# Kernel optimization log

Hardware: AMD Instinct MI355X
Metric: run time of the kernel (lower is better)

## Reference

```python
import jax, jax.numpy as jnp
import numpy as np

D = 768      # d_model (hardcoded in module)
H = 12       # heads (ViT-Base)
HD = D // H  # head_dim = 64
FF = 4 * D   # mlp hidden = 3072
L = 32       # num_latents
B, N = 64, 197
EPS = 1e-6


def _ln(x, g, b):
    mu = jnp.mean(x, axis=-1, keepdims=True)
    var = jnp.mean(jnp.square(x - mu), axis=-1, keepdims=True)
    return (x - mu) * jax.lax.rsqrt(var + EPS) * g + b


def _attn_simple(q, k, v):
    # fusion attention: single-head, scale = C ** -0.5 over full dim
    C = q.shape[-1]
    a = jax.nn.softmax(jnp.einsum('bnc,bmc->bnm', q, k) * (C ** -0.5), axis=-1)
    return jnp.einsum('bnm,bmc->bnc', a, v)


def _mha(x, qkv_w, qkv_b, proj_w, proj_b):
    Bx, Nx, C = x.shape
    qkv = (x @ qkv_w + qkv_b).reshape(Bx, Nx, 3, H, HD)
    q, k, v = jnp.moveaxis(qkv, 2, 0)           # each [B, N, H, HD]
    scores = jnp.einsum('bnhd,bmhd->bhnm', q, k) * (HD ** -0.5)
    a = jax.nn.softmax(scores, axis=-1)
    out = jnp.einsum('bhnm,bmhd->bnhd', a, v).reshape(Bx, Nx, C)
    return out @ proj_w + proj_b


def _mlp(x, w1, b1, w2, b2):
    return jax.nn.gelu(x @ w1 + b1, approximate=False) @ w2 + b2


def setup_inputs() -> dict:
    key = jax.random.key(0)
    ks = iter(jax.random.split(key, 40))
    std = 0.02
    d = {
        'x': jax.random.normal(next(ks), (B, N, D), jnp.float32),
        'y': jax.random.normal(next(ks), (B, N, D), jnp.float32),
        'latents': jax.random.normal(next(ks), (1, L, D), jnp.float32) * std,
        'scale_a': jnp.zeros((1,), jnp.float32) + 0.1,
        'scale_v': jnp.zeros((1,), jnp.float32) + 0.1,
    }
    for p in ('p', 'm'):
        d[f'{p}_n1_g'] = jnp.ones((D,), jnp.float32)
        d[f'{p}_n1_b'] = jnp.zeros((D,), jnp.float32)
        d[f'{p}_qkv_w'] = jax.random.normal(next(ks), (D, 3 * D), jnp.float32) * std
        d[f'{p}_qkv_b'] = jnp.zeros((3 * D,), jnp.float32)
        d[f'{p}_proj_w'] = jax.random.normal(next(ks), (D, D), jnp.float32) * std
        d[f'{p}_proj_b'] = jnp.zeros((D,), jnp.float32)
        d[f'{p}_n2_g'] = jnp.ones((D,), jnp.float32)
        d[f'{p}_n2_b'] = jnp.zeros((D,), jnp.float32)
        d[f'{p}_fc1_w'] = jax.random.normal(next(ks), (D, FF), jnp.float32) * std
        d[f'{p}_fc1_b'] = jnp.zeros((FF,), jnp.float32)
        d[f'{p}_fc2_w'] = jax.random.normal(next(ks), (FF, D), jnp.float32) * std
        d[f'{p}_fc2_b'] = jnp.zeros((D,), jnp.float32)
    return d


def reference(x, y, latents, scale_a, scale_v,
              p_n1_g, p_n1_b, p_qkv_w, p_qkv_b, p_proj_w, p_proj_b,
              p_n2_g, p_n2_b, p_fc1_w, p_fc1_b, p_fc2_w, p_fc2_b,
              m_n1_g, m_n1_b, m_qkv_w, m_qkv_b, m_proj_w, m_proj_b,
              m_n2_g, m_n2_b, m_fc1_w, m_fc1_b, m_fc2_w, m_fc2_b):
    BS = x.shape[0]
    # ---- fusion: latent bottleneck cross-attention ----
    concat = jnp.concatenate([x, y], axis=1)                       # [B, 2N, D]
    lat = jnp.broadcast_to(latents, (BS, L, D))
    fused = _attn_simple(lat, concat, concat)                      # [B, L, D]
    x = x + scale_a * _attn_simple(x, fused, fused)
    y = y + scale_v * _attn_simple(y, fused, fused)
    # ---- pre-norm attn + MLP blocks ----
    x = x + _mha(_ln(x, p_n1_g, p_n1_b), p_qkv_w, p_qkv_b, p_proj_w, p_proj_b)
    y = y + _mha(_ln(y, m_n1_g, m_n1_b), m_qkv_w, m_qkv_b, m_proj_w, m_proj_b)
    x = x + _mlp(_ln(x, p_n2_g, p_n2_b), p_fc1_w, p_fc1_b, p_fc2_w, p_fc2_b)
    y = y + _mlp(_ln(y, m_n2_g, m_n2_b), m_fc1_w, m_fc1_b, m_fc2_w, m_fc2_b)
    return (x, y)
```

## Files before the change

### kernel.cpp

```cpp
#include <hip/hip_runtime.h>
#include <math.h>


namespace {

constexpr int BB = 64, NN = 197, DD = 768, HH = 12, HDIM = 64, FF = 3072, LL = 32;
constexpr int N2 = 2 * NN;
constexpr int ROWS = BB * NN;
constexpr float SCALE_D = 0.036084391824351615f;
constexpr float SCALE_H = 0.125f;

constexpr long long B_AHI    = 0;
constexpr long long B_ALO    = 19365888;
constexpr long long B_GHI    = 40894464;
constexpr long long B_GLO    = 118358016;
constexpr long long B_CONCAT = 0;
constexpr long long B_SCORES = 0;
constexpr long long B_QKV    = 125829120;
constexpr long long B_FUSED  = 242221056;
constexpr long long B_S1T    = 248512512;
constexpr long long B_A2     = 252706816;
constexpr long long B_S2     = 256901120;
constexpr long long B_P1     = 258998272;
constexpr long long B_WHI    = 297795584;
constexpr long long B_WLO    = 303038464;

__device__ inline ushort f2bf(float f) {
  unsigned x = __float_as_uint(f);
  unsigned r = (x + 0x7FFFu + ((x >> 16) & 1u)) >> 16;
  return (ushort)r;
}
__device__ inline float bf2f(ushort u) {
  return __uint_as_float(((unsigned)u) << 16);
}

using bf16x8v = __attribute__((ext_vector_type(8))) short;
using f32x4v  = __attribute__((ext_vector_type(4))) float;

enum { ME_BIAS = 0, ME_RESID_BIAS = 1, ME_GELU_SPLIT = 2 };

struct MP {
  const ushort* Ah; const ushort* Al; int lda;
  const ushort* Wh; const ushort* Wl; int ldw;
  float* C; int ldc;
  const float* bias;
  const float* R; int ldr;
  ushort* Oh; ushort* Ol; int ldo;
  int M, N, K;
};

template <int EPI>
__global__ __launch_bounds__(256, 2) void mgemm_k(MP p) {
  __shared__ ushort sAh[128 * 40], sAl[128 * 40], sBh[128 * 40], sBl[128 * 40];
  const int tid = threadIdx.x;
  const int m0 = blockIdx.y * 128, n0 = blockIdx.x * 128;
  const int l = tid & 63, w = tid >> 6;
  const int wm = (w >> 1) * 64, wn = (w & 1) * 64;
  const int fr = l & 15, fq = l >> 4;

  f32x4v acc[4][4];
#pragma unroll
  for (int i = 0; i < 4; ++i)
#pragma unroll
    for (int j = 0; j < 4; ++j)
#pragma unroll
      for (int r = 0; r < 4; ++r) acc[i][j][r] = 0.f;

  const int srow = tid >> 2;
  const int skg  = tid & 3;

  for (int k0 = 0; k0 < p.K; k0 += 32) {
#pragma unroll
    for (int pass = 0; pass < 2; ++pass) {
      const int row = srow + pass * 64;
      const int lo_off = row * 40 + skg * 8;
      {
        const int mg = m0 + row;
        uint4 vh = make_uint4(0, 0, 0, 0), vl = make_uint4(0, 0, 0, 0);
        if (mg < p.M) {
          const long long off = (long long)mg * p.lda + k0 + skg * 8;
          vh = *reinterpret_cast<const uint4*>(p.Ah + off);
          vl = *reinterpret_cast<const uint4*>(p.Al + off);
        }
        *reinterpret_cast<uint4*>(&sAh[lo_off]) = vh;
        *reinterpret_cast<uint4*>(&sAl[lo_off]) = vl;
      }
      {
        const int ng = n0 + row;
        const long long off = (long long)ng * p.ldw + k0 + skg * 8;
        *reinterpret_cast<uint4*>(&sBh[lo_off]) =
            *reinterpret_cast<const uint4*>(p.Wh + off);
        *reinterpret_cast<uint4*>(&sBl[lo_off]) =
            *reinterpret_cast<const uint4*>(p.Wl + off);
      }
    }
    __syncthreads();

    bf16x8v ah[4], al[4];
#pragma unroll
    for (int mi = 0; mi < 4; ++mi) {
      const int ro = (wm + mi * 16 + fr) * 40 + fq * 8;
      ah[mi] = *reinterpret_cast<const bf16x8v*>(&sAh[ro]);
      al[mi] = *reinterpret_cast<const bf16x8v*>(&sAl[ro]);
    }
#pragma unroll
    for (int ni = 0; ni < 4; ++ni) {
      const int ro = (wn + ni * 16 + fr) * 40 + fq * 8;
      const bf16x8v bh = *reinterpret_cast<const bf16x8v*>(&sBh[ro]);
      const bf16x8v bl = *reinterpret_cast<const bf16x8v*>(&sBl[ro]);
#pragma unroll
      for (int mi = 0; mi < 4; ++mi) {
        acc[mi][ni] = __builtin_amdgcn_mfma_f32_16x16x32_bf16(al[mi], bh, acc[mi][ni], 0, 0, 0);
        acc[mi][ni] = __builtin_amdgcn_mfma_f32_16x16x32_bf16(ah[mi], bl, acc[mi][ni], 0, 0, 0);
        acc[mi][ni] = __builtin_amdgcn_mfma_f32_16x16x32_bf16(ah[mi], bh, acc[mi][ni], 0, 0, 0);
      }
    }
    __syncthreads();
  }

#pragma unroll
  for (int mi = 0; mi < 4; ++mi) {
    const int rb = m0 + wm + mi * 16 + fq * 4;
#pragma unroll
    for (int ni = 0; ni < 4; ++ni) {
      const int col = n0 + wn + ni * 16 + fr;
#pragma unroll
      for (int r = 0; r < 4; ++r) {
        const int mg = rb + r;
        if (mg >= p.M) continue;
        float v = acc[mi][ni][r];
        if (EPI == ME_BIAS) {
          p.C[(long long)mg * p.ldc + col] = v + p.bias[col];
        } else if (EPI == ME_RESID_BIAS) {
          p.C[(long long)mg * p.ldc + col] =
              v + p.bias[col] + p.R[(long long)mg * p.ldr + col];
        } else {
          v += p.bias[col];
          v = 0.5f * v * (1.f + erff(v * 0.70710678118654752f));
          const ushort h = f2bf(v);
          const long long o = (long long)mg * p.ldo + col;
          p.Oh[o] = h;
          p.Ol[o] = f2bf(v - bf2f(h));
        }
      }
    }
  }
}

template <int EPI>
static void launch_mgemm(hipStream_t st, const MP& p) {
  dim3 grid(p.N / 128, (p.M + 127) / 128);
  hipLaunchKernelGGL(HIP_KERNEL_NAME(mgemm_k<EPI>), grid, dim3(256), 0, st, p);
}

struct GemmP {
  const float* A; long long sA1, sA2; int lda;
  const float* W; long long sW1, sW2; int ldw;
  float*       C; long long sC1, sC2; int ldc;
  const float* R; long long sR1, sR2; int ldr;
  const float* bias;
  const float* scaleptr;
  int M, N, K, Z2;
  float alpha;
};

enum { E_NONE = 0, E_BIAS = 1, E_RESID_SCALE = 4 };

template <int BM, int BN, int BK, int TM, int TN, bool WT, int EPI>
__global__ __launch_bounds__(256) void gemm_k(GemmP p) {
  constexpr int NX = BN / TN;
  __shared__ float As[BK][BM + 4];
  __shared__ float Ws[BK][BN + 4];

  const int tid = threadIdx.x;
  const int z = blockIdx.z;
  const int z1 = z / p.Z2, z2 = z % p.Z2;
  const float* A = p.A + (long long)z1 * p.sA1 + (long long)z2 * p.sA2;
  const float* W = p.W + (long long)z1 * p.sW1 + (long long)z2 * p.sW2;
  float*       C = p.C + (long long)z1 * p.sC1 + (long long)z2 * p.sC2;
  const float* R = p.R ? p.R + (long long)z1 * p.sR1 + (long long)z2 * p.sR2 : nullptr;

  const int m0 = blockIdx.y * BM;
  const int n0 = blockIdx.x * BN;
  const int tx = tid % NX;
  const int ty = tid / NX;

  float acc[TM][TN];
#pragma unroll
  for (int i = 0; i < TM; ++i)
#pragma unroll
    for (int j = 0; j < TN; ++j) acc[i][j] = 0.f;

  for (int k0 = 0; k0 < p.K; k0 += BK) {
    for (int l = tid; l < BM * BK; l += 256) {
      const int m = l / BK, kc = l % BK;
      const int mg = m0 + m, kg = k0 + kc;
      float v = 0.f;
      if (mg < p.M && kg < p.K) v = A[(long long)mg * p.lda + kg];
      As[kc][m] = v;
    }
    if (!WT) {
      for (int l = tid; l < BK * BN; l += 256) {
        const int kc = l / BN, n = l % BN;
        const int ng = n0 + n, kg = k0 + kc;
        float v = 0.f;
        if (ng < p.N && kg < p.K) v = W[(long long)kg * p.ldw + ng];
        Ws[kc][n] = v;
      }
    } else {
      for (int l = tid; l < BK * BN; l += 256) {
        const int n = l / BK, kc = l % BK;
        const int ng = n0 + n, kg = k0 + kc;
        float v = 0.f;
        if (ng < p.N && kg < p.K) v = W[(long long)ng * p.ldw + kg];
        Ws[kc][n] = v;
      }
    }
    __syncthreads();

#pragma unroll
    for (int kk = 0; kk < BK; ++kk) {
      float af[TM], wf[TN];
#pragma unroll
      for (int i = 0; i < TM; i += 4) {
        const float4 t = *reinterpret_cast<const float4*>(&As[kk][ty * TM + i]);
        af[i] = t.x; af[i + 1] = t.y; af[i + 2] = t.z; af[i + 3] = t.w;
      }
#pragma unroll
      for (int j = 0; j < TN; j += 4) {
        const float4 t = *reinterpret_cast<const float4*>(&Ws[kk][tx * TN + j]);
        wf[j] = t.x; wf[j + 1] = t.y; wf[j + 2] = t.z; wf[j + 3] = t.w;
      }
#pragma unroll
      for (int i = 0; i < TM; ++i)
#pragma unroll
        for (int j = 0; j < TN; ++j) acc[i][j] += af[i] * wf[j];
    }
    __syncthreads();
  }

  float sc = 0.f;
  if (EPI == E_RESID_SCALE) sc = p.scaleptr[0];
#pragma unroll
  for (int i = 0; i < TM; ++i) {
    const int mg = m0 + ty * TM + i;
    if (mg >= p.M) continue;
#pragma unroll
    for (int j = 0; j < TN; ++j) {
      const int ng = n0 + tx * TN + j;
      if (ng >= p.N) continue;
      float v = acc[i][j];
      if (EPI == E_NONE) v *= p.alpha;
      if (EPI == E_BIAS) v += p.bias[ng];
      if (EPI == E_RESID_SCALE) v = R[(long long)mg * p.ldr + ng] + sc * v;
      C[(long long)mg * p.ldc + ng] = v;
    }
  }
}

template <int BM, int BN, int BK, int TM, int TN, bool WT, int EPI>
static void launch_gemm(hipStream_t st, const GemmP& p, int Z) {
  dim3 grid((p.N + BN - 1) / BN, (p.M + BM - 1) / BM, Z);
  hipLaunchKernelGGL(HIP_KERNEL_NAME(gemm_k<BM, BN, BK, TM, TN, WT, EPI>),
                     grid, dim3(256), 0, st, p);
}


__global__ __launch_bounds__(256) void concat_k(const float* __restrict__ x,
                                                const float* __restrict__ y,
                                                float* __restrict__ c) {
  const long long total4 = (long long)BB * N2 * DD / 4;
  const long long i = (long long)blockIdx.x * 256 + threadIdx.x;
  if (i >= total4) return;
  const long long e = i * 4;
  const int b = (int)(e / ((long long)N2 * DD));
  const long long rem = e % ((long long)N2 * DD);
  const int r = (int)(rem / DD);
  const int col = (int)(rem % DD);
  const float* src = (r < NN) ? (x + ((long long)b * NN + r) * DD + col)
                              : (y + ((long long)b * NN + (r - NN)) * DD + col);
  reinterpret_cast<float4*>(c)[i] = *reinterpret_cast<const float4*>(src);
}

__global__ __launch_bounds__(256) void ln_split_k(const float* __restrict__ in,
                                                  ushort* __restrict__ oh,
                                                  ushort* __restrict__ ol,
                                                  const float* __restrict__ g,
                                                  const float* __restrict__ b) {
  const int row = blockIdx.x;
  const int tid = threadIdx.x;
  const float* src = in + (long long)row * DD;
  const float v0 = src[tid], v1 = src[tid + 256], v2 = src[tid + 512];
  __shared__ float red[4];
  const int wid = tid >> 6;

  float s = v0 + v1 + v2;
#pragma unroll
  for (int o = 32; o; o >>= 1) s += __shfl_xor(s, o);
  if ((tid & 63) == 0) red[wid] = s;
  __syncthreads();
  const float mu = (red[0] + red[1] + red[2] + red[3]) * (1.f / 768.f);
  const float d0 = v0 - mu, d1 = v1 - mu, d2 = v2 - mu;
  __syncthreads();

  float q = d0 * d0 + d1 * d1 + d2 * d2;
#pragma unroll
  for (int o = 32; o; o >>= 1) q += __shfl_xor(q, o);
  if ((tid & 63) == 0) red[wid] = q;
  __syncthreads();
  const float var = (red[0] + red[1] + red[2] + red[3]) * (1.f / 768.f);
  const float rs = 1.f / sqrtf(var + 1e-6f);

  ushort* dh = oh + (long long)row * DD;
  ushort* dl = ol + (long long)row * DD;
#pragma unroll
  for (int c = 0; c < 3; ++c) {
    const int idx = tid + c * 256;
    const float dv = (c == 0 ? d0 : c == 1 ? d1 : d2);
    const float v = dv * rs * g[idx] + b[idx];
    const ushort h = f2bf(v);
    dh[idx] = h;
    dl[idx] = f2bf(v - bf2f(h));
  }
}

__global__ __launch_bounds__(256) void split_k(const float* __restrict__ in,
                                               ushort* __restrict__ oh,
                                               ushort* __restrict__ ol,
                                               long long n4) {
  const long long i = (long long)blockIdx.x * 256 + threadIdx.x;
  if (i >= n4) return;
  const float4 v = reinterpret_cast<const float4*>(in)[i];
  ushort4 h, lo;
  h.x = f2bf(v.x); lo.x = f2bf(v.x - bf2f(h.x));
  h.y = f2bf(v.y); lo.y = f2bf(v.y - bf2f(h.y));
  h.z = f2bf(v.z); lo.z = f2bf(v.z - bf2f(h.z));
  h.w = f2bf(v.w); lo.w = f2bf(v.w - bf2f(h.w));
  reinterpret_cast<ushort4*>(oh)[i] = h;
  reinterpret_cast<ushort4*>(ol)[i] = lo;
}

__global__ __launch_bounds__(256) void wsplit_k(const float* __restrict__ W,
                                                ushort* __restrict__ th,
                                                ushort* __restrict__ tl,
                                                int K, int N) {
  __shared__ float t[32][33];
  const int tid = threadIdx.x;
  const int kb = blockIdx.y * 32, nb = blockIdx.x * 32;
  for (int u = tid; u < 1024; u += 256) {
    const int k = u >> 5, n = u & 31;
    t[k][n] = W[(long long)(kb + k) * N + nb + n];
  }
  __syncthreads();
  const int n = tid >> 3, k4 = tid & 7;
  ushort4 vh, vl;
  {
    float v;
    v = t[k4 * 4 + 0][n]; vh.x = f2bf(v); vl.x = f2bf(v - bf2f(vh.x));
    v = t[k4 * 4 + 1][n]; vh.y = f2bf(v); vl.y = f2bf(v - bf2f(vh.y));
    v = t[k4 * 4 + 2][n]; vh.z = f2bf(v); vl.z = f2bf(v - bf2f(vh.z));
    v = t[k4 * 4 + 3][n]; vh.w = f2bf(v); vl.w = f2bf(v - bf2f(vh.w));
  }
  const long long o = (long long)(nb + n) * K + kb + k4 * 4;
  *reinterpret_cast<ushort4*>(th + o) = vh;
  *reinterpret_cast<ushort4*>(tl + o) = vl;
}

__global__ __launch_bounds__(256) void sm1_k(const float* __restrict__ S1t,
                                             float* __restrict__ A2) {
  const int b = blockIdx.x >> 5, l = blockIdx.x & 31;
  const int tid = threadIdx.x;
  const float* src = S1t + (long long)b * N2 * LL + l;
  const bool has2 = (tid + 256) < N2;
  const float v0 = src[(long long)tid * LL];
  const float v1 = has2 ? src[(long long)(tid + 256) * LL] : -3.0e38f;

  __shared__ float red[4];
  const int wid = tid >> 6;
  float mx = fmaxf(v0, v1);
#pragma unroll
  for (int o = 32; o; o >>= 1) mx = fmaxf(mx, __shfl_xor(mx, o));
  if ((tid & 63) == 0) red[wid] = mx;
  __syncthreads();
  mx = fmaxf(fmaxf(red[0], red[1]), fmaxf(red[2], red[3]));
  __syncthreads();

  const float p0 = expf(v0 - mx);
  const float p1 = has2 ? expf(v1 - mx) : 0.f;
  float s = p0 + p1;
#pragma unroll
  for (int o = 32; o; o >>= 1) s += __shfl_xor(s, o);
  if ((tid & 63) == 0) red[wid] = s;
  __syncthreads();
  const float inv = 1.f / (red[0] + red[1] + red[2] + red[3]);

  float* dst = A2 + (long long)b * LL * N2 + (long long)l * N2;
  dst[tid] = p0 * inv;
  if (has2) dst[tid + 256] = p1 * inv;
}

__global__ __launch_bounds__(256) void sm2_k(float* __restrict__ S, int rows) {
  const long long i = (long long)blockIdx.x * 256 + threadIdx.x;
  if (i >= rows) return;
  float* r = S + i * 32;
  float v[32];
  const float4* r4 = reinterpret_cast<const float4*>(r);
#pragma unroll
  for (int j = 0; j < 8; ++j) {
    const float4 t = r4[j];
    v[4 * j] = t.x; v[4 * j + 1] = t.y; v[4 * j + 2] = t.z; v[4 * j + 3] = t.w;
  }
  float mx = v[0];
#pragma unroll
  for (int j = 1; j < 32; ++j) mx = fmaxf(mx, v[j]);
  float s = 0.f;
#pragma unroll
  for (int j = 0; j < 32; ++j) { v[j] = expf(v[j] - mx); s += v[j]; }
  const float inv = 1.f / s;
  float4* w4 = reinterpret_cast<float4*>(r);
#pragma unroll
  for (int j = 0; j < 8; ++j) {
    float4 t;
    t.x = v[4 * j] * inv; t.y = v[4 * j + 1] * inv;
    t.z = v[4 * j + 2] * inv; t.w = v[4 * j + 3] * inv;
    w4[j] = t;
  }
}

__global__ __launch_bounds__(256) void smS_k(float* __restrict__ S, long long rows) {
  const int lane = threadIdx.x & 63;
  const long long row = (long long)blockIdx.x * 4 + (threadIdx.x >> 6);
  if (row >= rows) return;
  float* r = S + row * NN;
  float v[4];
#pragma unroll
  for (int j = 0; j < 4; ++j) {
    const int idx = lane + j * 64;
    v[j] = (idx < NN) ? r[idx] : -3.0e38f;
  }
  float mx = fmaxf(fmaxf(v[0], v[1]), fmaxf(v[2], v[3]));
#pragma unroll
  for (int o = 32; o; o >>= 1) mx = fmaxf(mx, __shfl_xor(mx, o));
  float pv[4];
  float s = 0.f;
#pragma unroll
  for (int j = 0; j < 4; ++j) {
    const int idx = lane + j * 64;
    pv[j] = (idx < NN) ? expf(v[j] - mx) : 0.f;
    s += pv[j];
  }
#pragma unroll
  for (int o = 32; o; o >>= 1) s += __shfl_xor(s, o);
  const float inv = 1.f / s;
#pragma unroll
  for (int j = 0; j < 4; ++j) {
    const int idx = lane + j * 64;
    if (idx < NN) r[idx] = pv[j] * inv;
  }
}

static GemmP mk(const float* A, long long sA1, long long sA2, int lda,
                const float* W, long long sW1, long long sW2, int ldw,
                float* C, long long sC1, long long sC2, int ldc,
                int M, int N, int K, int Z2, float alpha,
                const float* bias = nullptr,
                const float* R = nullptr, long long sR1 = 0, long long sR2 = 0, int ldr = 0,
                const float* scaleptr = nullptr) {
  GemmP p;
  p.A = A; p.sA1 = sA1; p.sA2 = sA2; p.lda = lda;
  p.W = W; p.sW1 = sW1; p.sW2 = sW2; p.ldw = ldw;
  p.C = C; p.sC1 = sC1; p.sC2 = sC2; p.ldc = ldc;
  p.R = R; p.sR1 = sR1; p.sR2 = sR2; p.ldr = ldr;
  p.bias = bias; p.scaleptr = scaleptr;
  p.M = M; p.N = N; p.K = K; p.Z2 = Z2; p.alpha = alpha;
  return p;
}

static MP mkm(const ushort* Ah, const ushort* Al, int lda,
              const ushort* Wh, const ushort* Wl, int ldw,
              int M, int N, int K, const float* bias,
              float* C = nullptr, int ldc = 0,
              const float* R = nullptr, int ldr = 0,
              ushort* Oh = nullptr, ushort* Ol = nullptr, int ldo = 0) {
  MP p;
  p.Ah = Ah; p.Al = Al; p.lda = lda;
  p.Wh = Wh; p.Wl = Wl; p.ldw = ldw;
  p.C = C; p.ldc = ldc; p.bias = bias;
  p.R = R; p.ldr = ldr;
  p.Oh = Oh; p.Ol = Ol; p.ldo = ldo;
  p.M = M; p.N = N; p.K = K;
  return p;
}

}

extern "C" void kernel_launch(void* const* d_in, const int* in_sizes, int n_in,
                              void* d_out, int out_size, void* d_ws, size_t ws_size,
                              hipStream_t stream) {
  const float* x   = (const float*)d_in[0];
  const float* y   = (const float*)d_in[1];
  const float* lat = (const float*)d_in[2];
  const float* scale_a = (const float*)d_in[3];
  const float* scale_v = (const float*)d_in[4];
  const float* PRM[2][12];
  for (int i = 0; i < 12; ++i) {
    PRM[0][i] = (const float*)d_in[5 + i];
    PRM[1][i] = (const float*)d_in[17 + i];
  }

  char* ws = (char*)d_ws;
  ushort* Ahi = (ushort*)(ws + B_AHI);
  ushort* Alo = (ushort*)(ws + B_ALO);
  ushort* Ghi = (ushort*)(ws + B_GHI);
  ushort* Glo = (ushort*)(ws + B_GLO);
  float* concat = (float*)(ws + B_CONCAT);
  float* scores = (float*)(ws + B_SCORES);
  float* qkv    = (float*)(ws + B_QKV);
  float* fused  = (float*)(ws + B_FUSED);
  float* S1t    = (float*)(ws + B_S1T);
  float* A2     = (float*)(ws + B_A2);
  float* S2     = (float*)(ws + B_S2);
  float* P1     = (float*)(ws + B_P1);
  ushort* Whi   = (ushort*)(ws + B_WHI);
  ushort* Wlo   = (ushort*)(ws + B_WLO);

  float* outX = (float*)d_out;
  float* outY = outX + (long long)ROWS * DD;

  {
    const long long tot4 = (long long)BB * N2 * DD / 4;
    concat_k<<<(unsigned)((tot4 + 255) / 256), 256, 0, stream>>>(x, y, concat);
  }
  launch_gemm<128, 32, 8, 4, 4, true, E_NONE>(
      stream,
      mk(concat, (long long)N2 * DD, 0, DD,
         lat, 0, 0, DD,
         S1t, (long long)N2 * LL, 0, LL,
         N2, LL, DD, 1, SCALE_D),
      BB);
  sm1_k<<<BB * LL, 256, 0, stream>>>(S1t, A2);
  launch_gemm<32, 128, 8, 4, 4, false, E_NONE>(
      stream,
      mk(A2, (long long)LL * N2, 0, N2,
         concat, (long long)N2 * DD, 0, DD,
         fused, (long long)LL * DD, 0, DD,
         LL, DD, N2, 1, 1.f),
      BB);
  for (int s = 0; s < 2; ++s) {
    const float* q = s == 0 ? x : y;
    const float* sp = s == 0 ? scale_a : scale_v;
    float* out = s == 0 ? outX : outY;
    launch_gemm<128, 32, 8, 4, 4, true, E_NONE>(
        stream,
        mk(q, (long long)NN * DD, 0, DD,
           fused, (long long)LL * DD, 0, DD,
           S2, (long long)NN * LL, 0, LL,
           NN, LL, DD, 1, SCALE_D),
        BB);
    sm2_k<<<(BB * NN + 255) / 256, 256, 0, stream>>>(S2, BB * NN);
    launch_gemm<128, 128, 8, 8, 8, false, E_RESID_SCALE>(
        stream,
        mk(S2, (long long)NN * LL, 0, LL,
           fused, (long long)LL * DD, 0, DD,
           out, (long long)NN * DD, 0, DD,
           NN, DD, LL, 1, 1.f,
           nullptr,
           q, (long long)NN * DD, 0, DD,
           sp),
        BB);
  }

  const long long splitN4 = (long long)ROWS * DD / 4;
  for (int s = 0; s < 2; ++s) {
    float* out = s == 0 ? outX : outY;
    const float* const* pp = PRM[s];
    const float *n1g = pp[0], *n1b = pp[1], *qkvw = pp[2], *qkvb = pp[3],
                *projw = pp[4], *projb = pp[5], *n2g = pp[6], *n2b = pp[7],
                *fc1w = pp[8], *fc1b = pp[9], *fc2w = pp[10], *fc2b = pp[11];

    ln_split_k<<<ROWS, 256, 0, stream>>>(out, Ahi, Alo, n1g, n1b);
    wsplit_k<<<dim3(3 * DD / 32, DD / 32), 256, 0, stream>>>(qkvw, Whi, Wlo, DD, 3 * DD);
    launch_mgemm<ME_BIAS>(stream,
        mkm(Ahi, Alo, DD, Whi, Wlo, DD, ROWS, 3 * DD, DD, qkvb, qkv, 3 * DD));
    launch_gemm<128, 128, 8, 8, 8, true, E_NONE>(
        stream,
        mk(qkv + 0 * DD, (long long)NN * 3 * DD, HDIM, 3 * DD,
           qkv + 1 * DD, (long long)NN * 3 * DD, HDIM, 3 * DD,
           scores, (long long)HH * NN * NN, (long long)NN * NN, NN,
           NN, NN, HDIM, HH, SCALE_H),
        BB * HH);
    smS_k<<<(unsigned)(((long long)BB * HH * NN + 3) / 4), 256, 0, stream>>>(
        scores, (long long)BB * HH * NN);
    launch_gemm<128, 64, 8, 8, 4, false, E_NONE>(
        stream,
        mk(scores, (long long)HH * NN * NN, (long long)NN * NN, NN,
           qkv + 2 * DD, (long long)NN * 3 * DD, HDIM, 3 * DD,
           P1, (long long)NN * DD, HDIM, DD,
           NN, HDIM, NN, HH, 1.f),
        BB * HH);
    split_k<<<(unsigned)((splitN4 + 255) / 256), 256, 0, stream>>>(P1, Ahi, Alo, splitN4);
    wsplit_k<<<dim3(DD / 32, DD / 32), 256, 0, stream>>>(projw, Whi, Wlo, DD, DD);
    launch_mgemm<ME_RESID_BIAS>(stream,
        mkm(Ahi, Alo, DD, Whi, Wlo, DD, ROWS, DD, DD, projb, out, DD, out, DD));
    ln_split_k<<<ROWS, 256, 0, stream>>>(out, Ahi, Alo, n2g, n2b);
    wsplit_k<<<dim3(FF / 32, DD / 32), 256, 0, stream>>>(fc1w, Whi, Wlo, DD, FF);
    launch_mgemm<ME_GELU_SPLIT>(stream,
        mkm(Ahi, Alo, DD, Whi, Wlo, DD, ROWS, FF, DD, fc1b,
            nullptr, 0, nullptr, 0, Ghi, Glo, FF));
    wsplit_k<<<dim3(DD / 32, FF / 32), 256, 0, stream>>>(fc2w, Whi, Wlo, FF, DD);
    launch_mgemm<ME_RESID_BIAS>(stream,
        mkm(Ghi, Glo, FF, Whi, Wlo, FF, ROWS, DD, FF, fc2b, out, DD, out, DD));
  }
}
```

Before: 3.120 ms.

## Use global_load_lds with XCD-aware tile remap in split-bf16 GEMM; fuse PV split

The split-bf16 MFMA GEMM now loads its A/B tiles straight into LDS with global_load_lds, one wave per operand buffer. Rows are clamped rather than zero-filled, and the 40-element LDS padding is dropped, which allows three workgroups per CU. Tiles are remapped from a 1D grid so that consecutive tiles share an XCD, aiming for better L2 reuse. The attention PV GEMM now writes hi/lo bf16 outputs directly, removing the separate fp32 write and split kernel. The risk is that unpadded LDS rows may cause bank conflicts on the fragment reads.

```diff
diff --git a/kernel.cpp b/kernel.cpp
--- a/kernel.cpp
+++ b/kernel.cpp
@@ -21,7 +21,8 @@
 constexpr long long B_S1T    = 248512512;
 constexpr long long B_A2     = 252706816;
 constexpr long long B_S2     = 256901120;
-constexpr long long B_P1     = 258998272;
+constexpr long long B_PHI    = 258998272;
+constexpr long long B_PLO    = 278364160;
 constexpr long long B_WHI    = 297795584;
 constexpr long long B_WLO    = 303038464;
 
@@ -47,65 +48,66 @@
   const float* R; int ldr;
   ushort* Oh; ushort* Ol; int ldo;
   int M, N, K;
+  int nxb, nwg;
 };
 
 template <int EPI>
-__global__ __launch_bounds__(256, 2) void mgemm_k(MP p) {
-  __shared__ ushort sAh[128 * 40], sAl[128 * 40], sBh[128 * 40], sBl[128 * 40];
+__global__ __launch_bounds__(256, 3) void mgemm_k(MP p) {
+  __shared__ ushort sAh[128 * 32], sAl[128 * 32], sBh[128 * 32], sBl[128 * 32];
   const int tid = threadIdx.x;
-  const int m0 = blockIdx.y * 128, n0 = blockIdx.x * 128;
+
+  const int nwg = p.nwg;
+  const int h = blockIdx.x;
+  const int q = nwg >> 3, r = nwg & 7;
+  const int xcd = h & 7, ii = h >> 3;
+  const int wg = (xcd < r ? xcd * (q + 1) : r * (q + 1) + (xcd - r) * q) + ii;
+  const int m0 = (wg / p.nxb) * 128;
+  const int n0 = (wg % p.nxb) * 128;
+
   const int l = tid & 63, w = tid >> 6;
   const int wm = (w >> 1) * 64, wn = (w & 1) * 64;
   const int fr = l & 15, fq = l >> 4;
 
+  ushort* const lbuf = (w == 0) ? sAh : (w == 1) ? sAl : (w == 2) ? sBh : sBl;
+  const ushort* const gsrc = (w == 0) ? p.Ah : (w == 1) ? p.Al
+                            : (w == 2) ? p.Wh : p.Wl;
+  const int ldg   = (w < 2) ? p.lda : p.ldw;
+  const int rbase = (w < 2) ? m0 : n0;
+  const int rlim  = ((w < 2) ? p.M : p.N) - 1;
+  const int rl = l >> 2;
+  const int ch = l & 3;
+
   f32x4v acc[4][4];
 #pragma unroll
   for (int i = 0; i < 4; ++i)
 #pragma unroll
     for (int j = 0; j < 4; ++j)
 #pragma unroll
-      for (int r = 0; r < 4; ++r) acc[i][j][r] = 0.f;
-
-  const int srow = tid >> 2;
-  const int skg  = tid & 3;
+      for (int t = 0; t < 4; ++t) acc[i][j][t] = 0.f;
 
   for (int k0 = 0; k0 < p.K; k0 += 32) {
 #pragma unroll
-    for (int pass = 0; pass < 2; ++pass) {
-      const int row = srow + pass * 64;
-      const int lo_off = row * 40 + skg * 8;
-      {
-        const int mg = m0 + row;
-        uint4 vh = make_uint4(0, 0, 0, 0), vl = make_uint4(0, 0, 0, 0);
-        if (mg < p.M) {
-          const long long off = (long long)mg * p.lda + k0 + skg * 8;
-          vh = *reinterpret_cast<const uint4*>(p.Ah + off);
-          vl = *reinterpret_cast<const uint4*>(p.Al + off);
-        }
-        *reinterpret_cast<uint4*>(&sAh[lo_off]) = vh;
-        *reinterpret_cast<uint4*>(&sAl[lo_off]) = vl;
-      }
-      {
-        const int ng = n0 + row;
-        const long long off = (long long)ng * p.ldw + k0 + skg * 8;
-        *reinterpret_cast<uint4*>(&sBh[lo_off]) =
-            *reinterpret_cast<const uint4*>(p.Wh + off);
-        *reinterpret_cast<uint4*>(&sBl[lo_off]) =
-            *reinterpret_cast<const uint4*>(p.Wl + off);
-      }
+    for (int j = 0; j < 8; ++j) {
+      int rg = rbase + j * 16 + rl;
+      rg = rg > rlim ? rlim : rg;
+      const ushort* gp = gsrc + (long long)rg * ldg + k0 + ch * 8;
+      __builtin_amdgcn_global_load_lds(
+          (const __attribute__((address_space(1))) void*)gp,
+          (__attribute__((address_space(3))) void*)(lbuf + j * 512),
+          16, 0, 0);
     }
     __syncthreads();
 
     bf16x8v ah[4], al[4];
 #pragma unroll
     for (int mi = 0; mi < 4; ++mi) {
-      const int ro = (wm + mi * 16 + fr) * 40 + fq * 8;
+      const int ro = (wm + mi * 16 + fr) * 32 + fq * 8;
       ah[mi] = *reinterpret_cast<const bf16x8v*>(&sAh[ro]);
       al[mi] = *reinterpret_cast<const bf16x8v*>(&sAl[ro]);
     }
 #pragma unroll
     for (int ni = 0; ni < 4; ++ni) {
-      const int ro = (wn + ni * 16 + fr) * 40 + fq * 8;
+      const int ro = (wn + ni * 16 + fr) * 32 + fq * 8;
       const bf16x8v bh = *reinterpret_cast<const bf16x8v*>(&sBh[ro]);
       const bf16x8v bl = *reinterpret_cast<const bf16x8v*>(&sBl[ro]);
 #pragma unroll
@@ -125,10 +127,10 @@
     for (int ni = 0; ni < 4; ++ni) {
       const int col = n0 + wn + ni * 16 + fr;
 #pragma unroll
-      for (int r = 0; r < 4; ++r) {
-        const int mg = rb + r;
+      for (int t = 0; t < 4; ++t) {
+        const int mg = rb + t;
         if (mg >= p.M) continue;
-        float v = acc[mi][ni][r];
+        float v = acc[mi][ni][t];
         if (EPI == ME_BIAS) {
           p.C[(long long)mg * p.ldc + col] = v + p.bias[col];
         } else if (EPI == ME_RESID_BIAS) {
@@ -137,10 +139,10 @@
         } else {
           v += p.bias[col];
           v = 0.5f * v * (1.f + erff(v * 0.70710678118654752f));
-          const ushort h = f2bf(v);
+          const ushort hh = f2bf(v);
           const long long o = (long long)mg * p.ldo + col;
-          p.Oh[o] = h;
-          p.Ol[o] = f2bf(v - bf2f(h));
+          p.Oh[o] = hh;
+          p.Ol[o] = f2bf(v - bf2f(hh));
         }
       }
     }
@@ -148,9 +150,10 @@
 }
 
 template <int EPI>
-static void launch_mgemm(hipStream_t st, const MP& p) {
-  dim3 grid(p.N / 128, (p.M + 127) / 128);
-  hipLaunchKernelGGL(HIP_KERNEL_NAME(mgemm_k<EPI>), grid, dim3(256), 0, st, p);
+static void launch_mgemm(hipStream_t st, MP p) {
+  p.nxb = p.N / 128;
+  p.nwg = p.nxb * ((p.M + 127) / 128);
+  hipLaunchKernelGGL(HIP_KERNEL_NAME(mgemm_k<EPI>), dim3(p.nwg), dim3(256), 0, st, p);
 }
 
 struct GemmP {
@@ -160,11 +163,12 @@
   const float* R; long long sR1, sR2; int ldr;
   const float* bias;
   const float* scaleptr;
+  ushort* Oh; ushort* Ol;
   int M, N, K, Z2;
   float alpha;
 };
 
-enum { E_NONE = 0, E_BIAS = 1, E_RESID_SCALE = 4 };
+enum { E_NONE = 0, E_BIAS = 1, E_RESID_SCALE = 4, E_SPLIT = 5 };
 
 template <int BM, int BN, int BK, int TM, int TN, bool WT, int EPI>
 __global__ __launch_bounds__(256) void gemm_k(GemmP p) {
@@ -177,8 +181,10 @@
   const int z1 = z / p.Z2, z2 = z % p.Z2;
   const float* A = p.A + (long long)z1 * p.sA1 + (long long)z2 * p.sA2;
   const float* W = p.W + (long long)z1 * p.sW1 + (long long)z2 * p.sW2;
-  float*       C = p.C + (long long)z1 * p.sC1 + (long long)z2 * p.sC2;
+  float*       C = p.C ? p.C + (long long)z1 * p.sC1 + (long long)z2 * p.sC2 : nullptr;
   const float* R = p.R ? p.R + (long long)z1 * p.sR1 + (long long)z2 * p.sR2 : nullptr;
+  ushort* Oh = p.Oh ? p.Oh + (long long)z1 * p.sC1 + (long long)z2 * p.sC2 : nullptr;
+  ushort* Ol = p.Ol ? p.Ol + (long long)z1 * p.sC1 + (long long)z2 * p.sC2 : nullptr;
 
   const int m0 = blockIdx.y * BM;
   const int n0 = blockIdx.x * BN;
@@ -253,7 +259,14 @@
       if (EPI == E_NONE) v *= p.alpha;
       if (EPI == E_BIAS) v += p.bias[ng];
       if (EPI == E_RESID_SCALE) v = R[(long long)mg * p.ldr + ng] + sc * v;
-      C[(long long)mg * p.ldc + ng] = v;
+      if (EPI == E_SPLIT) {
+        const long long o = (long long)mg * p.ldc + ng;
+        const ushort hh = f2bf(v);
+        Oh[o] = hh;
+        Ol[o] = f2bf(v - bf2f(hh));
+      } else {
+        C[(long long)mg * p.ldc + ng] = v;
+      }
     }
   }
 }
@@ -303,10 +316,10 @@
   const float d0 = v0 - mu, d1 = v1 - mu, d2 = v2 - mu;
   __syncthreads();
 
-  float q = d0 * d0 + d1 * d1 + d2 * d2;
-#pragma unroll
-  for (int o = 32; o; o >>= 1) q += __shfl_xor(q, o);
-  if ((tid & 63) == 0) red[wid] = q;
+  float qv = d0 * d0 + d1 * d1 + d2 * d2;
+#pragma unroll
+  for (int o = 32; o; o >>= 1) qv += __shfl_xor(qv, o);
+  if ((tid & 63) == 0) red[wid] = qv;
   __syncthreads();
   const float var = (red[0] + red[1] + red[2] + red[3]) * (1.f / 768.f);
   const float rs = 1.f / sqrtf(var + 1e-6f);
@@ -318,26 +331,10 @@
     const int idx = tid + c * 256;
     const float dv = (c == 0 ? d0 : c == 1 ? d1 : d2);
     const float v = dv * rs * g[idx] + b[idx];
-    const ushort h = f2bf(v);
-    dh[idx] = h;
-    dl[idx] = f2bf(v - bf2f(h));
-  }
-}
-
-__global__ __launch_bounds__(256) void split_k(const float* __restrict__ in,
-                                               ushort* __restrict__ oh,
-                                               ushort* __restrict__ ol,
-                                               long long n4) {
-  const long long i = (long long)blockIdx.x * 256 + threadIdx.x;
-  if (i >= n4) return;
-  const float4 v = reinterpret_cast<const float4*>(in)[i];
-  ushort4 h, lo;
-  h.x = f2bf(v.x); lo.x = f2bf(v.x - bf2f(h.x));
-  h.y = f2bf(v.y); lo.y = f2bf(v.y - bf2f(h.y));
-  h.z = f2bf(v.z); lo.z = f2bf(v.z - bf2f(h.z));
-  h.w = f2bf(v.w); lo.w = f2bf(v.w - bf2f(h.w));
-  reinterpret_cast<ushort4*>(oh)[i] = h;
-  reinterpret_cast<ushort4*>(ol)[i] = lo;
+    const ushort hh = f2bf(v);
+    dh[idx] = hh;
+    dl[idx] = f2bf(v - bf2f(hh));
+  }
 }
 
 __global__ __launch_bounds__(256) void wsplit_k(const float* __restrict__ W,
@@ -472,6 +469,7 @@
   p.C = C; p.sC1 = sC1; p.sC2 = sC2; p.ldc = ldc;
   p.R = R; p.sR1 = sR1; p.sR2 = sR2; p.ldr = ldr;
   p.bias = bias; p.scaleptr = scaleptr;
+  p.Oh = nullptr; p.Ol = nullptr;
   p.M = M; p.N = N; p.K = K; p.Z2 = Z2; p.alpha = alpha;
   return p;
 }
@@ -489,6 +487,7 @@
   p.R = R; p.ldr = ldr;
   p.Oh = Oh; p.Ol = Ol; p.ldo = ldo;
   p.M = M; p.N = N; p.K = K;
+  p.nxb = 0; p.nwg = 0;
   return p;
 }
 
@@ -520,7 +519,8 @@
   float* S1t    = (float*)(ws + B_S1T);
   float* A2     = (float*)(ws + B_A2);
   float* S2     = (float*)(ws + B_S2);
-  float* P1     = (float*)(ws + B_P1);
+  ushort* Phi   = (ushort*)(ws + B_PHI);
+  ushort* Plo   = (ushort*)(ws + B_PLO);
   ushort* Whi   = (ushort*)(ws + B_WHI);
   ushort* Wlo   = (ushort*)(ws + B_WLO);
 
@@ -547,12 +547,12 @@
          LL, DD, N2, 1, 1.f),
       BB);
   for (int s = 0; s < 2; ++s) {
-    const float* q = s == 0 ? x : y;
+    const float* qq = s == 0 ? x : y;
     const float* sp = s == 0 ? scale_a : scale_v;
     float* out = s == 0 ? outX : outY;
     launch_gemm<128, 32, 8, 4, 4, true, E_NONE>(
         stream,
-        mk(q, (long long)NN * DD, 0, DD,
+        mk(qq, (long long)NN * DD, 0, DD,
            fused, (long long)LL * DD, 0, DD,
            S2, (long long)NN * LL, 0, LL,
            NN, LL, DD, 1, SCALE_D),
@@ -565,12 +565,11 @@
            out, (long long)NN * DD, 0, DD,
            NN, DD, LL, 1, 1.f,
            nullptr,
-           q, (long long)NN * DD, 0, DD,
+           qq, (long long)NN * DD, 0, DD,
            sp),
         BB);
   }
 
-  const long long splitN4 = (long long)ROWS * DD / 4;
   for (int s = 0; s < 2; ++s) {
     float* out = s == 0 ? outX : outY;
     const float* const* pp = PRM[s];
@@ -591,17 +590,17 @@
         BB * HH);
     smS_k<<<(unsigned)(((long long)BB * HH * NN + 3) / 4), 256, 0, stream>>>(
         scores, (long long)BB * HH * NN);
-    launch_gemm<128, 64, 8, 8, 4, false, E_NONE>(
-        stream,
-        mk(scores, (long long)HH * NN * NN, (long long)NN * NN, NN,
-           qkv + 2 * DD, (long long)NN * 3 * DD, HDIM, 3 * DD,
-           P1, (long long)NN * DD, HDIM, DD,
-           NN, HDIM, NN, HH, 1.f),
-        BB * HH);
-    split_k<<<(unsigned)((splitN4 + 255) / 256), 256, 0, stream>>>(P1, Ahi, Alo, splitN4);
+    {
+      GemmP pv = mk(scores, (long long)HH * NN * NN, (long long)NN * NN, NN,
+                    qkv + 2 * DD, (long long)NN * 3 * DD, HDIM, 3 * DD,
+                    nullptr, (long long)NN * DD, HDIM, DD,
+                    NN, HDIM, NN, HH, 1.f);
+      pv.Oh = Phi; pv.Ol = Plo;
+      launch_gemm<128, 64, 8, 8, 4, false, E_SPLIT>(stream, pv, BB * HH);
+    }
     wsplit_k<<<dim3(DD / 32, DD / 32), 256, 0, stream>>>(projw, Whi, Wlo, DD, DD);
     launch_mgemm<ME_RESID_BIAS>(stream,
-        mkm(Ahi, Alo, DD, Whi, Wlo, DD, ROWS, DD, DD, projb, out, DD, out, DD));
+        mkm(Phi, Plo, DD, Whi, Wlo, DD, ROWS, DD, DD, projb, out, DD, out, DD));
     ln_split_k<<<ROWS, 256, 0, stream>>>(out, Ahi, Alo, n2g, n2b);
     wsplit_k<<<dim3(FF / 32, DD / 32), 256, 0, stream>>>(fc1w, Whi, Wlo, DD, FF);
     launch_mgemm<ME_GELU_SPLIT>(stream,
```

After: 3.020 ms. 3.2% less time.
